# Performance work log

Measured on AMD Instinct MI355X. Metric: run time of the kernel, lower is better.

The kernel has to match this reference:

```python
import jax, jax.numpy as jnp
import numpy as np

K = 9
PAD = K // 2


def setup_inputs() -> dict:
    key = jax.random.key(0)
    k1, k2 = jax.random.split(key)
    H, W = 1024, 1024
    unet_out = jax.random.normal(k1, (H, W, 3), dtype=jnp.float32)
    cnn_out = jax.random.uniform(k2, (H, W, K * K), dtype=jnp.float32)
    return {"unet_out": unet_out, "cnn_out": cnn_out}


def reference(unet_out, cnn_out):
    # unet_out: [H, W, 3]; cnn_out: [H, W, 81] per-pixel 9x9 kernels
    H, W, C = unet_out.shape
    padded = jnp.pad(unet_out, ((PAD, PAD), (PAD, PAD), (0, 0)), mode="reflect")
    # Gather 9x9 neighborhoods as shifted static slices; index order ki*K+kj
    # matches F.unfold's (kernel_row, kernel_col) layout.
    patches = jnp.stack(
        [padded[i:i + H, j:j + W, :] for i in range(K) for j in range(K)],
        axis=2,
    )  # [H, W, 81, 3]
    out = jnp.einsum("hwkc,hwk->hwc", patches, cnn_out)  # [H, W, 3]
    return out
```

## Files before the change

### kernel.cpp

```cpp
#include <hip/hip_runtime.h>

#define HH 1024
#define WW 1024
#define KK 9
#define PADK 4
#define TSX 16
#define TSY 8
#define NPX 128
#define TROWS 16
#define TCOLS 24
#define NW 81
#define ROWB 5184

#define GLDS(src, dst, w)                                              \
  __builtin_amdgcn_global_load_lds(                                    \
      (const __attribute__((address_space(1))) unsigned int*)(src),    \
      (__attribute__((address_space(3))) unsigned int*)(dst), w, 0, 0)

__global__ __launch_bounds__(128) void denoiser_kpn(
    const float* __restrict__ unet, const float* __restrict__ cnn,
    float* __restrict__ out) {
  __shared__ __attribute__((aligned(16))) float wlds[NPX * NW];
  __shared__ float4 tile[TROWS][TCOLS + 1];

  const int tid = threadIdx.x;
  const int lane = tid & 63;
  const int wv = tid >> 6;
  const int tx = tid & 15;
  const int ty = tid >> 4;
  const int px0 = blockIdx.x * TSX;
  const int py0 = blockIdx.y * TSY;

  float tr_[3][3];
#pragma unroll
  for (int i = 0; i < 3; ++i) {
    const int idx = tid + 128 * i;
    const int r = idx / TCOLS;
    const int c = idx - r * TCOLS;
    int gy = py0 - PADK + r;
    gy = gy < 0 ? -gy : (gy >= HH ? 2 * HH - 2 - gy : gy);
    int gx = px0 - PADK + c;
    gx = gx < 0 ? -gx : (gx >= WW ? 2 * WW - 2 - gx : gx);
    __builtin_memcpy(&tr_[i][0], unet + ((size_t)gy * WW + gx) * 3, 12);
  }
  __builtin_amdgcn_sched_barrier(0);

#pragma unroll
  for (int rr = 0; rr < 4; ++rr) {
    const int r = wv * 4 + rr;
    const char* s = (const char*)(cnn + ((size_t)(py0 + r) * WW + px0) * NW);
    char* d = (char*)wlds + r * ROWB;
#pragma unroll
    for (int i = 0; i < 5; ++i)
      GLDS(s + i * 1024 + lane * 16, d + i * 1024 + lane * 16, 16);
    if (lane < 16) GLDS(s + 5120 + lane * 4, d + 5120 + lane * 4, 4);
  }
  __builtin_amdgcn_sched_barrier(0);

#pragma unroll
  for (int i = 0; i < 3; ++i) {
    const int idx = tid + 128 * i;
    const int r = idx / TCOLS;
    const int c = idx - r * TCOLS;
    tile[r][c] = make_float4(tr_[i][0], tr_[i][1], tr_[i][2], 0.0f);
  }
  __builtin_amdgcn_sched_barrier(0);
  asm volatile("s_waitcnt lgkmcnt(0)" ::: "memory");
  __builtin_amdgcn_s_barrier();
  __builtin_amdgcn_sched_barrier(0);
  asm volatile("s_waitcnt vmcnt(0)" ::: "memory");
  __builtin_amdgcn_sched_barrier(0);

  float ax = 0.0f, ay = 0.0f, az = 0.0f;
  const float* wrow = wlds + tid * NW;
#pragma unroll
  for (int ki = 0; ki < KK; ++ki)
#pragma unroll
    for (int kj = 0; kj < KK; ++kj) {
      const float4 pv = tile[ty + ki][tx + kj];
      const float w = wrow[ki * KK + kj];
      ax = fmaf(w, pv.x, ax);
      ay = fmaf(w, pv.y, ay);
      az = fmaf(w, pv.z, az);
    }

  const float o[3] = {ax, ay, az};
  __builtin_memcpy(out + ((size_t)(py0 + ty) * WW + px0 + tx) * 3, &o[0], 12);
}

extern "C" void kernel_launch(void* const* d_in, const int* in_sizes, int n_in,
                              void* d_out, int out_size, void* d_ws, size_t ws_size,
                              hipStream_t stream) {
  const float* unet = (const float*)d_in[0];
  const float* cnn = (const float*)d_in[1];
  float* out = (float*)d_out;
  dim3 grid(WW / TSX, HH / TSY);
  dim3 block(NPX);
  denoiser_kpn<<<grid, block, 0, stream>>>(unet, cnn, out);
}
```

Baseline: 71.41 us.

## Double-buffer per-row weight DMA and split each pixel's 81 taps across four lanes

Weight loading is reorganised into two-row chunks streamed through a double-buffered LDS area, so compute on one chunk overlaps the global-to-LDS DMA of the next, and LDS use per block drops. Each pixel's 81-tap dot product is split across 4 lanes of about 20 taps each, reduced with xor shuffles, which gives four compute phases per block. The tile stride changes to reduce LDS bank conflicts. The cost is extra shuffles, hand-tuned vmcnt waits that must match the DMA count exactly, and a missing workgroup barrier between phases, so cross-wave buffer reuse could race.

```diff
diff --git a/kernel.cpp b/kernel.cpp
--- a/kernel.cpp
+++ b/kernel.cpp
@@ -6,30 +6,72 @@
 #define PADK 4
 #define TSX 16
 #define TSY 8
-#define NPX 128
 #define TROWS 16
 #define TCOLS 24
+#define TSTR 26
 #define NW 81
-#define ROWB 5184
+#define CHF 2592
+#define HALF 1296
 
 #define GLDS(src, dst, w)                                              \
   __builtin_amdgcn_global_load_lds(                                    \
       (const __attribute__((address_space(1))) unsigned int*)(src),    \
       (__attribute__((address_space(3))) unsigned int*)(dst), w, 0, 0)
 
+#define SBAR __builtin_amdgcn_sched_barrier(0)
+
 __global__ __launch_bounds__(128) void denoiser_kpn(
     const float* __restrict__ unet, const float* __restrict__ cnn,
     float* __restrict__ out) {
-  __shared__ __attribute__((aligned(16))) float wlds[NPX * NW];
-  __shared__ float4 tile[TROWS][TCOLS + 1];
+  __shared__ float4 tile[TROWS][TSTR];
+  __shared__ float wlds[2][CHF];
 
   const int tid = threadIdx.x;
   const int lane = tid & 63;
   const int wv = tid >> 6;
-  const int tx = tid & 15;
-  const int ty = tid >> 4;
+  const int q = tid >> 2;
+  const int jj = tid & 3;
+  const int tx = q & 15;
   const int px0 = blockIdx.x * TSX;
   const int py0 = blockIdx.y * TSY;
+
+  auto wdma = [&](int c, int buf) {
+    const char* s =
+        (const char*)(cnn + ((size_t)((py0 + 2 * c + wv) * WW + px0)) * NW);
+    char* d = (char*)&wlds[buf][wv * HALF];
+#pragma unroll
+    for (int i = 0; i < 5; ++i)
+      GLDS(s + i * 1024 + lane * 16, d + i * 1024 + lane * 16, 16);
+    if (lane < 4) GLDS(s + 5120 + lane * 16, d + 5120 + lane * 16, 16);
+  };
+
+  auto do_phase = [&](const float* wb, int trow, int gy) {
+    float ax = 0.f, ay = 0.f, az = 0.f;
+    int kj = 2 * jj;
+    int tidx = (trow + 2 * jj) * TSTR + tx + kj;
+#pragma unroll
+    for (int n = 0; n < 21; ++n) {
+      if (n < 20 || jj == 3) {
+        const float4 pv = ((const float4*)tile)[tidx];
+        const float w = wb[n];
+        ax = fmaf(w, pv.x, ax);
+        ay = fmaf(w, pv.y, ay);
+        az = fmaf(w, pv.z, az);
+      }
+      ++kj;
+      ++tidx;
+      const bool wrap = (kj == KK);
+      kj = wrap ? 0 : kj;
+      tidx += wrap ? (TSTR - KK) : 0;
+    }
+    ax += __shfl_xor(ax, 1); ax += __shfl_xor(ax, 2);
+    ay += __shfl_xor(ay, 1); ay += __shfl_xor(ay, 2);
+    az += __shfl_xor(az, 1); az += __shfl_xor(az, 2);
+    if (jj == 0) {
+      const float o[3] = {ax, ay, az};
+      __builtin_memcpy(out + ((size_t)gy * WW + px0 + tx) * 3, &o[0], 12);
+    }
+  };
 
   float tr_[3][3];
 #pragma unroll
@@ -43,20 +85,10 @@
     gx = gx < 0 ? -gx : (gx >= WW ? 2 * WW - 2 - gx : gx);
     __builtin_memcpy(&tr_[i][0], unet + ((size_t)gy * WW + gx) * 3, 12);
   }
-  __builtin_amdgcn_sched_barrier(0);
-
-#pragma unroll
-  for (int rr = 0; rr < 4; ++rr) {
-    const int r = wv * 4 + rr;
-    const char* s = (const char*)(cnn + ((size_t)(py0 + r) * WW + px0) * NW);
-    char* d = (char*)wlds + r * ROWB;
-#pragma unroll
-    for (int i = 0; i < 5; ++i)
-      GLDS(s + i * 1024 + lane * 16, d + i * 1024 + lane * 16, 16);
-    if (lane < 16) GLDS(s + 5120 + lane * 4, d + 5120 + lane * 4, 4);
-  }
-  __builtin_amdgcn_sched_barrier(0);
-
+  SBAR;
+  wdma(0, 0);
+  wdma(1, 1);
+  SBAR;
 #pragma unroll
   for (int i = 0; i < 3; ++i) {
     const int idx = tid + 128 * i;
@@ -64,28 +96,32 @@
     const int c = idx - r * TCOLS;
     tile[r][c] = make_float4(tr_[i][0], tr_[i][1], tr_[i][2], 0.0f);
   }
-  __builtin_amdgcn_sched_barrier(0);
+  SBAR;
   asm volatile("s_waitcnt lgkmcnt(0)" ::: "memory");
   __builtin_amdgcn_s_barrier();
-  __builtin_amdgcn_sched_barrier(0);
-  asm volatile("s_waitcnt vmcnt(0)" ::: "memory");
-  __builtin_amdgcn_sched_barrier(0);
+  SBAR;
 
-  float ax = 0.0f, ay = 0.0f, az = 0.0f;
-  const float* wrow = wlds + tid * NW;
-#pragma unroll
-  for (int ki = 0; ki < KK; ++ki)
-#pragma unroll
-    for (int kj = 0; kj < KK; ++kj) {
-      const float4 pv = tile[ty + ki][tx + kj];
-      const float w = wrow[ki * KK + kj];
-      ax = fmaf(w, pv.x, ax);
-      ay = fmaf(w, pv.y, ay);
-      az = fmaf(w, pv.z, az);
-    }
+  const int wb0 = q * NW + 20 * jj;
 
-  const float o[3] = {ax, ay, az};
-  __builtin_memcpy(out + ((size_t)(py0 + ty) * WW + px0 + tx) * 3, &o[0], 12);
+  asm volatile("s_waitcnt vmcnt(6)" ::: "memory");
+  SBAR;
+  do_phase(&wlds[0][wb0], 0 + wv, py0 + 0 + wv);
+  SBAR;
+  wdma(2, 0);
+  SBAR;
+  asm volatile("s_waitcnt vmcnt(7)" ::: "memory");
+  SBAR;
+  do_phase(&wlds[1][wb0], 2 + wv, py0 + 2 + wv);
+  SBAR;
+  wdma(3, 1);
+  SBAR;
+  asm volatile("s_waitcnt vmcnt(7)" ::: "memory");
+  SBAR;
+  do_phase(&wlds[0][wb0], 4 + wv, py0 + 4 + wv);
+  SBAR;
+  asm volatile("s_waitcnt vmcnt(1)" ::: "memory");
+  SBAR;
+  do_phase(&wlds[1][wb0], 6 + wv, py0 + 6 + wv);
 }
 
 extern "C" void kernel_launch(void* const* d_in, const int* in_sizes, int n_in,
@@ -95,6 +131,6 @@
   const float* cnn = (const float*)d_in[1];
   float* out = (float*)d_out;
   dim3 grid(WW / TSX, HH / TSY);
-  dim3 block(NPX);
+  dim3 block(128);
   denoiser_kpn<<<grid, block, 0, stream>>>(unet, cnn, out);
 }
```

New measurement: 72.15 us. No clear change (+1.0%).

## Process 16x16 tiles in two phases, overlapping second weight load with compute

Applied to the files above, without the earlier changes.

Each 128-thread block now covers a 16x16 output tile and computes two pixels per thread in two 8-row phases. The per-pixel weights for both phases are issued as direct-to-LDS loads up front. A partial vmcnt wait lets the first phase's FMAs run while the second phase's weights are still arriving. The larger tile also shares a 24x24 image halo, which lowers redundant halo reads. The cost is roughly double the LDS per block, which lowers the number of resident blocks per CU for a kernel that is mostly bandwidth-bound.

```diff
diff --git a/kernel.cpp b/kernel.cpp
--- a/kernel.cpp
+++ b/kernel.cpp
@@ -5,23 +5,26 @@
 #define KK 9
 #define PADK 4
 #define TSX 16
-#define TSY 8
-#define NPX 128
-#define TROWS 16
+#define TSY 16
+#define TROWS 24
 #define TCOLS 24
+#define TSTR 25
 #define NW 81
 #define ROWB 5184
+#define SLOTF 5184
 
 #define GLDS(src, dst, w)                                              \
   __builtin_amdgcn_global_load_lds(                                    \
       (const __attribute__((address_space(1))) unsigned int*)(src),    \
       (__attribute__((address_space(3))) unsigned int*)(dst), w, 0, 0)
 
+#define SBAR __builtin_amdgcn_sched_barrier(0)
+
 __global__ __launch_bounds__(128) void denoiser_kpn(
     const float* __restrict__ unet, const float* __restrict__ cnn,
     float* __restrict__ out) {
-  __shared__ __attribute__((aligned(16))) float wlds[NPX * NW];
-  __shared__ float4 tile[TROWS][TCOLS + 1];
+  __shared__ __attribute__((aligned(16))) float wlds[2][2][SLOTF];
+  __shared__ float4 tile[TROWS][TSTR];
 
   const int tid = threadIdx.x;
   const int lane = tid & 63;
@@ -31,61 +34,85 @@
   const int px0 = blockIdx.x * TSX;
   const int py0 = blockIdx.y * TSY;
 
-  float tr_[3][3];
+  float tr_[5][3];
 #pragma unroll
-  for (int i = 0; i < 3; ++i) {
-    const int idx = tid + 128 * i;
-    const int r = idx / TCOLS;
-    const int c = idx - r * TCOLS;
+  for (int i = 0; i < 5; ++i) {
+    int e = tid + 128 * i;
+    if (e > 575) e = 575;
+    const int r = e / TCOLS;
+    const int c = e - r * TCOLS;
     int gy = py0 - PADK + r;
     gy = gy < 0 ? -gy : (gy >= HH ? 2 * HH - 2 - gy : gy);
     int gx = px0 - PADK + c;
     gx = gx < 0 ? -gx : (gx >= WW ? 2 * WW - 2 - gx : gx);
     __builtin_memcpy(&tr_[i][0], unet + ((size_t)gy * WW + gx) * 3, 12);
   }
-  __builtin_amdgcn_sched_barrier(0);
+  SBAR;
 
 #pragma unroll
-  for (int rr = 0; rr < 4; ++rr) {
-    const int r = wv * 4 + rr;
-    const char* s = (const char*)(cnn + ((size_t)(py0 + r) * WW + px0) * NW);
-    char* d = (char*)wlds + r * ROWB;
+  for (int ph = 0; ph < 2; ++ph)
 #pragma unroll
-    for (int i = 0; i < 5; ++i)
-      GLDS(s + i * 1024 + lane * 16, d + i * 1024 + lane * 16, 16);
-    if (lane < 16) GLDS(s + 5120 + lane * 4, d + 5120 + lane * 4, 4);
-  }
-  __builtin_amdgcn_sched_barrier(0);
+    for (int r = 0; r < 4; ++r) {
+      const int gr = py0 + ph * 8 + wv * 4 + r;
+      const char* s = (const char*)(cnn + ((size_t)gr * WW + px0) * NW);
+      char* d = (char*)&wlds[wv][ph][0] + r * ROWB;
+#pragma unroll
+      for (int i = 0; i < 5; ++i)
+        GLDS(s + i * 1024 + lane * 16, d + i * 1024 + lane * 16, 16);
+      if (lane < 4) GLDS(s + 5120 + lane * 16, d + 5120 + lane * 16, 16);
+    }
+  SBAR;
 
 #pragma unroll
-  for (int i = 0; i < 3; ++i) {
+  for (int i = 0; i < 5; ++i) {
     const int idx = tid + 128 * i;
-    const int r = idx / TCOLS;
-    const int c = idx - r * TCOLS;
-    tile[r][c] = make_float4(tr_[i][0], tr_[i][1], tr_[i][2], 0.0f);
+    if (idx < 576) {
+      const int r = idx / TCOLS;
+      const int c = idx - r * TCOLS;
+      tile[r][c] = make_float4(tr_[i][0], tr_[i][1], tr_[i][2], 0.0f);
+    }
   }
-  __builtin_amdgcn_sched_barrier(0);
+  SBAR;
   asm volatile("s_waitcnt lgkmcnt(0)" ::: "memory");
   __builtin_amdgcn_s_barrier();
-  __builtin_amdgcn_sched_barrier(0);
-  asm volatile("s_waitcnt vmcnt(0)" ::: "memory");
-  __builtin_amdgcn_sched_barrier(0);
+  SBAR;
 
-  float ax = 0.0f, ay = 0.0f, az = 0.0f;
-  const float* wrow = wlds + tid * NW;
+  const float* wrow = &wlds[wv][0][lane * NW];
+
+  asm volatile("s_waitcnt vmcnt(24)" ::: "memory");
+  SBAR;
+  float a0 = 0.f, a1 = 0.f, a2 = 0.f;
 #pragma unroll
   for (int ki = 0; ki < KK; ++ki)
 #pragma unroll
     for (int kj = 0; kj < KK; ++kj) {
       const float4 pv = tile[ty + ki][tx + kj];
       const float w = wrow[ki * KK + kj];
-      ax = fmaf(w, pv.x, ax);
-      ay = fmaf(w, pv.y, ay);
-      az = fmaf(w, pv.z, az);
+      a0 = fmaf(w, pv.x, a0);
+      a1 = fmaf(w, pv.y, a1);
+      a2 = fmaf(w, pv.z, a2);
+    }
+  SBAR;
+
+  asm volatile("s_waitcnt vmcnt(0)" ::: "memory");
+  SBAR;
+  const float* wrowB = &wlds[wv][1][lane * NW];
+  float b0 = 0.f, b1 = 0.f, b2 = 0.f;
+#pragma unroll
+  for (int ki = 0; ki < KK; ++ki)
+#pragma unroll
+    for (int kj = 0; kj < KK; ++kj) {
+      const float4 pv = tile[8 + ty + ki][tx + kj];
+      const float w = wrowB[ki * KK + kj];
+      b0 = fmaf(w, pv.x, b0);
+      b1 = fmaf(w, pv.y, b1);
+      b2 = fmaf(w, pv.z, b2);
     }
 
-  const float o[3] = {ax, ay, az};
-  __builtin_memcpy(out + ((size_t)(py0 + ty) * WW + px0 + tx) * 3, &o[0], 12);
+  const float oa[3] = {a0, a1, a2};
+  const float ob[3] = {b0, b1, b2};
+  __builtin_memcpy(out + ((size_t)(py0 + ty) * WW + px0 + tx) * 3, &oa[0], 12);
+  __builtin_memcpy(out + ((size_t)(py0 + 8 + ty) * WW + px0 + tx) * 3, &ob[0], 12);
 }
 
 extern "C" void kernel_launch(void* const* d_in, const int* in_sizes, int n_in,
@@ -95,6 +122,6 @@
   const float* cnn = (const float*)d_in[1];
   float* out = (float*)d_out;
   dim3 grid(WW / TSX, HH / TSY);
-  dim3 block(NPX);
+  dim3 block(128);
   denoiser_kpn<<<grid, block, 0, stream>>>(unet, cnn, out);
 }
```

After: 110.6 us. +54.9%, slower.

## Split weight loads into two chunks and overlap compute with second chunk

Applied to the files above, without the earlier changes.

Each wave now loads its four weight rows as two chunks of two rows. It waits only for the first chunk (vmcnt(12)) before computing, so the second chunk's global-to-LDS loads overlap with compute. Each pixel's 81 taps are split across a lane pair (36/45 taps) and combined with a shuffle, so 64 lanes handle 32 pixels per chunk. The tail load also changes from 4-byte to 16-byte transfers. This adds shuffles, an uneven lane workload and a write from only half the lanes, and relies on the hand-written vmcnt count matching the number of issued loads.

```diff
diff --git a/kernel.cpp b/kernel.cpp
--- a/kernel.cpp
+++ b/kernel.cpp
@@ -6,28 +6,31 @@
 #define PADK 4
 #define TSX 16
 #define TSY 8
-#define NPX 128
 #define TROWS 16
 #define TCOLS 24
+#define TSTR 25
 #define NW 81
 #define ROWB 5184
+#define CHUNKF 2592
 
 #define GLDS(src, dst, w)                                              \
   __builtin_amdgcn_global_load_lds(                                    \
       (const __attribute__((address_space(1))) unsigned int*)(src),    \
       (__attribute__((address_space(3))) unsigned int*)(dst), w, 0, 0)
 
+#define SBAR __builtin_amdgcn_sched_barrier(0)
+
 __global__ __launch_bounds__(128) void denoiser_kpn(
     const float* __restrict__ unet, const float* __restrict__ cnn,
     float* __restrict__ out) {
-  __shared__ __attribute__((aligned(16))) float wlds[NPX * NW];
-  __shared__ float4 tile[TROWS][TCOLS + 1];
+  __shared__ __attribute__((aligned(16))) float wlds[2][2][CHUNKF];
+  __shared__ float4 tile[TROWS][TSTR];
 
   const int tid = threadIdx.x;
   const int lane = tid & 63;
   const int wv = tid >> 6;
-  const int tx = tid & 15;
-  const int ty = tid >> 4;
+  const int p = lane >> 1;
+  const int h = lane & 1;
   const int px0 = blockIdx.x * TSX;
   const int py0 = blockIdx.y * TSY;
 
@@ -43,19 +46,21 @@
     gx = gx < 0 ? -gx : (gx >= WW ? 2 * WW - 2 - gx : gx);
     __builtin_memcpy(&tr_[i][0], unet + ((size_t)gy * WW + gx) * 3, 12);
   }
-  __builtin_amdgcn_sched_barrier(0);
+  SBAR;
 
 #pragma unroll
-  for (int rr = 0; rr < 4; ++rr) {
-    const int r = wv * 4 + rr;
-    const char* s = (const char*)(cnn + ((size_t)(py0 + r) * WW + px0) * NW);
-    char* d = (char*)wlds + r * ROWB;
+  for (int c = 0; c < 2; ++c)
 #pragma unroll
-    for (int i = 0; i < 5; ++i)
-      GLDS(s + i * 1024 + lane * 16, d + i * 1024 + lane * 16, 16);
-    if (lane < 16) GLDS(s + 5120 + lane * 4, d + 5120 + lane * 4, 4);
-  }
-  __builtin_amdgcn_sched_barrier(0);
+    for (int r = 0; r < 2; ++r) {
+      const int gr = py0 + wv * 4 + c * 2 + r;
+      const char* s = (const char*)(cnn + ((size_t)gr * WW + px0) * NW);
+      char* d = (char*)&wlds[wv][c][0] + r * ROWB;
+#pragma unroll
+      for (int i = 0; i < 5; ++i)
+        GLDS(s + i * 1024 + lane * 16, d + i * 1024 + lane * 16, 16);
+      if (lane < 4) GLDS(s + 5120 + lane * 16, d + 5120 + lane * 16, 16);
+    }
+  SBAR;
 
 #pragma unroll
   for (int i = 0; i < 3; ++i) {
@@ -64,28 +69,46 @@
     const int c = idx - r * TCOLS;
     tile[r][c] = make_float4(tr_[i][0], tr_[i][1], tr_[i][2], 0.0f);
   }
-  __builtin_amdgcn_sched_barrier(0);
+  SBAR;
   asm volatile("s_waitcnt lgkmcnt(0)" ::: "memory");
   __builtin_amdgcn_s_barrier();
-  __builtin_amdgcn_sched_barrier(0);
+  SBAR;
+
+  const int bcol = p & 15;
+  const int r0 = p >> 4;
+
+  auto do_chunk = [&](int c) {
+    const int brow = wv * 4 + c * 2 + r0;
+    const float* wb = &wlds[wv][c][p * NW + 36 * h];
+    const int tb = brow + (h ? 4 : 0);
+    float ax = 0.f, ay = 0.f, az = 0.f;
+#pragma unroll
+    for (int n = 0; n < 45; ++n) {
+      if (n < 36 || h) {
+        const float4 pv = tile[tb + n / 9][bcol + n % 9];
+        const float w = wb[n];
+        ax = fmaf(w, pv.x, ax);
+        ay = fmaf(w, pv.y, ay);
+        az = fmaf(w, pv.z, az);
+      }
+    }
+    ax += __shfl_xor(ax, 1);
+    ay += __shfl_xor(ay, 1);
+    az += __shfl_xor(az, 1);
+    if (h == 0) {
+      const float o[3] = {ax, ay, az};
+      __builtin_memcpy(out + ((size_t)(py0 + brow) * WW + px0 + bcol) * 3,
+                       &o[0], 12);
+    }
+  };
+
+  asm volatile("s_waitcnt vmcnt(12)" ::: "memory");
+  SBAR;
+  do_chunk(0);
+  SBAR;
   asm volatile("s_waitcnt vmcnt(0)" ::: "memory");
-  __builtin_amdgcn_sched_barrier(0);
-
-  float ax = 0.0f, ay = 0.0f, az = 0.0f;
-  const float* wrow = wlds + tid * NW;
-#pragma unroll
-  for (int ki = 0; ki < KK; ++ki)
-#pragma unroll
-    for (int kj = 0; kj < KK; ++kj) {
-      const float4 pv = tile[ty + ki][tx + kj];
-      const float w = wrow[ki * KK + kj];
-      ax = fmaf(w, pv.x, ax);
-      ay = fmaf(w, pv.y, ay);
-      az = fmaf(w, pv.z, az);
-    }
-
-  const float o[3] = {ax, ay, az};
-  __builtin_memcpy(out + ((size_t)(py0 + ty) * WW + px0 + tx) * 3, &o[0], 12);
+  SBAR;
+  do_chunk(1);
 }
 
 extern "C" void kernel_launch(void* const* d_in, const int* in_sizes, int n_in,
@@ -95,6 +118,6 @@
   const float* cnn = (const float*)d_in[1];
   float* out = (float*)d_out;
   dim3 grid(WW / TSX, HH / TSY);
-  dim3 block(NPX);
+  dim3 block(128);
   denoiser_kpn<<<grid, block, 0, stream>>>(unet, cnn, out);
 }
```

After: 76.55 us. +7.2%, slower.
